# Performance work log

Hardware: AMD Instinct MI355X
Metric: run time of the kernel (lower is better)

Reference implementation:

```python
import jax, jax.numpy as jnp
import numpy as np
from jax import lax

EPS = 1e-5

def conv2d(x, w, pad, dil):
    # x: NCHW, w: OIHW
    return lax.conv_general_dilated(
        x, w, window_strides=(1, 1), padding=[(pad, pad), (pad, pad)],
        rhs_dilation=(dil, dil), dimension_numbers=("NCHW", "OIHW", "NCHW"))

def batchnorm(x, gamma, beta):
    # training-mode BN: batch statistics over (N, H, W), biased variance
    m = x.mean(axis=(0, 2, 3), keepdims=True)
    v = x.var(axis=(0, 2, 3), keepdims=True)
    xh = (x - m) * lax.rsqrt(v + EPS)
    return gamma[None, :, None, None] * xh + beta[None, :, None, None]

def maxpool2(x):
    return lax.reduce_window(x, -jnp.inf, lax.max, (1, 1, 2, 2), (1, 1, 2, 2), "VALID")

def mhsa(x, wq, bq, wk, bk, wv, bv, rel_h, rel_w, heads=1):
    B, C, H, W = x.shape
    N = H * W
    d = C // heads
    q = (conv2d(x, wq, 0, 1) + bq[None, :, None, None]).reshape(B, heads, d, N)
    k = (conv2d(x, wk, 0, 1) + bk[None, :, None, None]).reshape(B, heads, d, N)
    v = (conv2d(x, wv, 0, 1) + bv[None, :, None, None]).reshape(B, heads, d, N)
    # content-content: q^T k -> [B, h, N, N]
    cc = jnp.einsum("bhdn,bhdm->bhnm", q, k)
    # content-position: (rel_h + rel_w) reshaped to [h, d, N], transposed, times q
    pos = (rel_h + rel_w).reshape(heads, d, N)  # broadcast-sum [1,h,d,1,H]+[1,h,d,W,1]
    cp = jnp.einsum("hnd,bhdm->bhnm", jnp.swapaxes(pos, 1, 2), q)
    attn = jax.nn.softmax(cc + cp, axis=-1)
    # out = v @ attn^T
    out = jnp.einsum("bhdn,bhmn->bhdm", v, attn)
    return out.reshape(B, C, H, W)


def setup_inputs() -> dict:
    key = jax.random.key(0)
    ks = jax.random.split(key, 16)
    B, in_ch, out_ch, S = 4, 128, 256, 64
    c4 = out_ch // 4  # 64 = MHSA channel dim
    w_scale = 0.05
    inp = {
        "x": jax.random.normal(ks[0], (B, in_ch, 2 * S, 2 * S), jnp.float32),
        "dc_w1": jax.random.normal(ks[1], (out_ch, in_ch, 3, 3), jnp.float32) * w_scale,
        "dc_b1": jnp.zeros((out_ch,), jnp.float32),
        "dc_g1": jnp.ones((out_ch,), jnp.float32),
        "dc_be1": jnp.zeros((out_ch,), jnp.float32),
        "dc_w2": jax.random.normal(ks[2], (out_ch, out_ch, 3, 3), jnp.float32) * w_scale,
        "dc_b2": jnp.zeros((out_ch,), jnp.float32),
        "dc_g2": jnp.ones((out_ch,), jnp.float32),
        "dc_be2": jnp.zeros((out_ch,), jnp.float32),
        "aspp1_w": jax.random.normal(ks[3], (c4, out_ch, 1, 1), jnp.float32) * w_scale,
        "aspp1_g": jnp.ones((c4,), jnp.float32),
        "aspp1_b": jnp.zeros((c4,), jnp.float32),
        "aspp2_w": jax.random.normal(ks[4], (c4, out_ch, 3, 3), jnp.float32) * w_scale,
        "aspp2_g": jnp.ones((c4,), jnp.float32),
        "aspp2_b": jnp.zeros((c4,), jnp.float32),
        "aspp3_w": jax.random.normal(ks[5], (c4, out_ch, 3, 3), jnp.float32) * w_scale,
        "aspp3_g": jnp.ones((c4,), jnp.float32),
        "aspp3_b": jnp.zeros((c4,), jnp.float32),
        "aspp4_w": jax.random.normal(ks[6], (c4, out_ch, 3, 3), jnp.float32) * w_scale,
        "aspp4_g": jnp.ones((c4,), jnp.float32),
        "aspp4_b": jnp.zeros((c4,), jnp.float32),
        "wq": jax.random.normal(ks[7], (c4, c4, 1, 1), jnp.float32) * w_scale,
        "bq": jnp.zeros((c4,), jnp.float32),
        "wk": jax.random.normal(ks[8], (c4, c4, 1, 1), jnp.float32) * w_scale,
        "bk": jnp.zeros((c4,), jnp.float32),
        "wv": jax.random.normal(ks[9], (c4, c4, 1, 1), jnp.float32) * w_scale,
        "bv": jnp.zeros((c4,), jnp.float32),
        "rel_h": jax.random.normal(ks[10], (1, 1, c4, 1, S), jnp.float32),
        "rel_w": jax.random.normal(ks[11], (1, 1, c4, S, 1), jnp.float32),
    }
    return inp


def reference(x, dc_w1, dc_b1, dc_g1, dc_be1, dc_w2, dc_b2, dc_g2, dc_be2,
              aspp1_w, aspp1_g, aspp1_b, aspp2_w, aspp2_g, aspp2_b,
              aspp3_w, aspp3_g, aspp3_b, aspp4_w, aspp4_g, aspp4_b,
              wq, bq, wk, bk, wv, bv, rel_h, rel_w):
    dilations = (1, 3, 6, 9)
    # mpconv: MaxPool2d(2) -> double_conv
    h = maxpool2(x)
    h = jax.nn.relu(batchnorm(conv2d(h, dc_w1, 1, 1) + dc_b1[None, :, None, None], dc_g1, dc_be1))
    h = jax.nn.relu(batchnorm(conv2d(h, dc_w2, 1, 1) + dc_b2[None, :, None, None], dc_g2, dc_be2))

    aspp = [(aspp1_w, aspp1_g, aspp1_b), (aspp2_w, aspp2_g, aspp2_b),
            (aspp3_w, aspp3_g, aspp3_b), (aspp4_w, aspp4_g, aspp4_b)]
    outs = []
    for (w, g, b), dil in zip(aspp, dilations):
        pad = 0 if dil == 1 else dil
        branch = jax.nn.relu(batchnorm(conv2d(h, w, pad, dil), g, b))
        outs.append(mhsa(branch, wq, bq, wk, bk, wv, bv, rel_h, rel_w))
    return jnp.concatenate(outs, axis=1)
```

## Files before the change

### kernel.cpp

```cpp
#include <hip/hip_runtime.h>
#include <math.h>

constexpr int Bn = 4;
constexpr int S  = 64;
constexpr int N  = 4096;

#define DEV static __device__ __forceinline__

typedef __attribute__((ext_vector_type(8))) short bf16x8;
typedef __attribute__((ext_vector_type(4))) float f32x4;

DEV unsigned short bfc(float x) {
  unsigned u = __float_as_uint(x);
  unsigned r = (u + 0x7FFFu + ((u >> 16) & 1u)) >> 16;
  return (unsigned short)r;
}

DEV void fma4(float4& a, float s, const float4 u) {
  a.x = fmaf(s, u.x, a.x); a.y = fmaf(s, u.y, a.y);
  a.z = fmaf(s, u.z, a.z); a.w = fmaf(s, u.w, a.w);
}

DEV void gload_lds16(const unsigned short* g, unsigned short* l) {
  __builtin_amdgcn_global_load_lds(
      (const __attribute__((address_space(1))) void*)g,
      (__attribute__((address_space(3))) void*)l, 16, 0, 0);
}

DEV void pswap32(unsigned& a, unsigned& b) {
  asm("v_permlane32_swap_b32 %0, %1" : "+v"(a), "+v"(b));
}
DEV void pswap16(unsigned& a, unsigned& b) {
  asm("v_permlane16_swap_b32 %0, %1" : "+v"(a), "+v"(b));
}

__global__ __launch_bounds__(256) void wtr_kernel(const float* __restrict__ src,
                                                  unsigned short* __restrict__ dst,
                                                  int Cout, int Cin, int T) {
  int i = blockIdx.x * 256 + threadIdx.x;
  int ci = i % Cin;
  int r  = i / Cin;
  int t  = r / Cout;
  int co = r - t * Cout;
  dst[i] = bfc(src[((size_t)co * Cin + ci) * T + t]);
}

__global__ __launch_bounds__(256) void pool_kernel(const float* __restrict__ x,
                                                   unsigned short* __restrict__ Pp1) {
  int i = blockIdx.x * 256 + threadIdx.x;
  int xg = i & 15, y = (i >> 4) & 63, c = (i >> 10) & 127, b = i >> 17;
  const float* s = x + (((size_t)(b * 128 + c) * 128) + 2 * y) * 128 + 8 * xg;
  float4 u0 = *(const float4*)(s), u1 = *(const float4*)(s + 4);
  float4 u2 = *(const float4*)(s + 128), u3 = *(const float4*)(s + 132);
  float m0 = fmaxf(fmaxf(u0.x, u0.y), fmaxf(u2.x, u2.y));
  float m1 = fmaxf(fmaxf(u0.z, u0.w), fmaxf(u2.z, u2.w));
  float m2 = fmaxf(fmaxf(u1.x, u1.y), fmaxf(u3.x, u3.y));
  float m3 = fmaxf(fmaxf(u1.z, u1.w), fmaxf(u3.z, u3.w));
  unsigned short* d = Pp1 + (((size_t)b * 66 + y + 1) * 66 + xg * 4 + 1) * 128 + c;
  d[0] = bfc(m0); d[128] = bfc(m1); d[256] = bfc(m2); d[384] = bfc(m3);
}

template <int CTOT>
__global__ __launch_bounds__(256) void dcconv_kernel(
    const unsigned short* __restrict__ in, const unsigned short* __restrict__ wt,
    float* __restrict__ out) {
  const int Wp = 66, CSEG = CTOT / 2;
  const int w = threadIdx.x >> 6, lane = threadIdx.x & 63;
  const int ln = lane & 15, quad = lane >> 4;
  const int b = blockIdx.z >> 1, h = blockIdx.z & 1, co0 = blockIdx.y * 64;
  const int n0 = blockIdx.x * 128 + w * 32;
  const unsigned short* inb = in + (size_t)b * Wp * Wp * CTOT + h * CSEG;
  const unsigned short* wth = wt + h * CSEG;
  float* outh = out + (size_t)h * 4 * 256 * N;
  size_t pix[2];
#pragma unroll
  for (int j = 0; j < 2; j++) {
    int n = n0 + j * 16 + ln;
    int y = n >> 6, x = n & 63;
    pix[j] = ((size_t)y * Wp + x) * CTOT;
  }
  f32x4 acc[4][2];
#pragma unroll
  for (int i = 0; i < 4; i++)
#pragma unroll
    for (int j = 0; j < 2; j++) acc[i][j] = (f32x4)(0.f);
#pragma unroll
  for (int ky = 0; ky < 3; ky++)
#pragma unroll
    for (int kx = 0; kx < 3; kx++) {
      const size_t toff = ((size_t)ky * Wp + kx) * CTOT;
      const unsigned short* wtap = wth + (size_t)(ky * 3 + kx) * 256 * CTOT;
      for (int kc = 0; kc < CSEG / 32; kc++) {
        const int ko = kc * 32 + quad * 8;
        bf16x8 a[4], bb[2];
#pragma unroll
        for (int i = 0; i < 4; i++)
          a[i] = *(const bf16x8*)(wtap + (size_t)(co0 + i * 16 + ln) * CTOT + ko);
#pragma unroll
        for (int j = 0; j < 2; j++)
          bb[j] = *(const bf16x8*)(inb + pix[j] + toff + ko);
#pragma unroll
        for (int i = 0; i < 4; i++)
#pragma unroll
          for (int j = 0; j < 2; j++)
            acc[i][j] = __builtin_amdgcn_mfma_f32_16x16x32_bf16(a[i], bb[j], acc[i][j], 0, 0, 0);
      }
    }
#pragma unroll
  for (int i = 0; i < 4; i++)
#pragma unroll
    for (int j = 0; j < 2; j++)
#pragma unroll
      for (int r = 0; r < 4; r++)
        outh[((size_t)(b * 256 + co0 + i * 16 + quad * 4 + r)) * N + n0 + j * 16 + ln] =
            acc[i][j][r];
}

__global__ __launch_bounds__(256) void branch_kernel(
    const unsigned short* __restrict__ in, const unsigned short* __restrict__ wtall,
    float* __restrict__ br) {
  const int Wp = 82, halo = 9, CIN = 256;
  const int w = threadIdx.x >> 6, lane = threadIdx.x & 63;
  const int ln = lane & 15, quad = lane >> 4;
  const int bb = blockIdx.y;
  const int kbr = bb >> 2, b = bb & 3;
  const int dil = (kbr == 0) ? 1 : 3 * kbr;
  const int klo = (kbr == 0) ? 1 : 0, khi = (kbr == 0) ? 2 : 3;
  const int hd = halo - dil;
  const int cw = (w & 1) * 32, nw = (w >> 1) * 32;
  const int n0 = blockIdx.x * 64 + nw;
  const unsigned short* inb = in + (size_t)b * Wp * Wp * CIN;
  size_t pix[2];
#pragma unroll
  for (int j = 0; j < 2; j++) {
    int n = n0 + j * 16 + ln;
    int y = n >> 6, x = n & 63;
    pix[j] = ((size_t)(y + hd) * Wp + x + hd) * CIN;
  }
  f32x4 acc[2][2];
#pragma unroll
  for (int i = 0; i < 2; i++)
#pragma unroll
    for (int j = 0; j < 2; j++) acc[i][j] = (f32x4)(0.f);
  for (int ky = klo; ky < khi; ky++)
    for (int kx = klo; kx < khi; kx++) {
      const size_t toff = ((size_t)ky * Wp + kx) * dil * CIN;
      const unsigned short* wtap =
          wtall + ((size_t)kbr * 9 + ky * 3 + kx) * 64 * CIN;
      for (int kc = 0; kc < CIN / 32; kc++) {
        const int ko = kc * 32 + quad * 8;
        bf16x8 a[2], bv[2];
#pragma unroll
        for (int i = 0; i < 2; i++)
          a[i] = *(const bf16x8*)(wtap + (size_t)(cw + i * 16 + ln) * CIN + ko);
#pragma unroll
        for (int j = 0; j < 2; j++)
          bv[j] = *(const bf16x8*)(inb + pix[j] + toff + ko);
#pragma unroll
        for (int i = 0; i < 2; i++)
#pragma unroll
          for (int j = 0; j < 2; j++)
            acc[i][j] = __builtin_amdgcn_mfma_f32_16x16x32_bf16(a[i], bv[j], acc[i][j], 0, 0, 0);
      }
    }
#pragma unroll
  for (int i = 0; i < 2; i++)
#pragma unroll
    for (int j = 0; j < 2; j++)
#pragma unroll
      for (int r = 0; r < 4; r++)
        br[((size_t)bb * 64 + cw + i * 16 + quad * 4 + r) * N + n0 + j * 16 + ln] =
            acc[i][j][r];
}

__global__ __launch_bounds__(256) void bn_stats_kernel(
    const float* __restrict__ t, const float* __restrict__ gamma,
    const float* __restrict__ beta, float* __restrict__ ss, int C) {
  const int c = blockIdx.x;
  float s = 0.f, s2 = 0.f;
  for (int b = 0; b < Bn; b++) {
    const float* p = t + ((size_t)(b * C + c)) * N;
    for (int i = threadIdx.x; i < N; i += 256) {
      float v = p[i];
      s += v; s2 = fmaf(v, v, s2);
    }
  }
  for (int off = 32; off; off >>= 1) {
    s += __shfl_down(s, off, 64);
    s2 += __shfl_down(s2, off, 64);
  }
  __shared__ float rs[4], rs2[4];
  const int wid = threadIdx.x >> 6, lane = threadIdx.x & 63;
  if (lane == 0) { rs[wid] = s; rs2[wid] = s2; }
  __syncthreads();
  if (threadIdx.x == 0) {
    float S1 = rs[0] + rs[1] + rs[2] + rs[3];
    float S2 = rs2[0] + rs2[1] + rs2[2] + rs2[3];
    const float cnt = (float)(Bn * N);
    float mean = S1 / cnt;
    float var = S2 / cnt - mean * mean;
    float sc = gamma[c] * rsqrtf(var + 1e-5f);
    ss[2 * c] = sc;
    ss[2 * c + 1] = beta[c] - mean * sc;
  }
}

__global__ __launch_bounds__(256) void bn_stats2_kernel(
    const float* __restrict__ ta, const float* __restrict__ tb,
    const float* __restrict__ gamma, const float* __restrict__ beta,
    float* __restrict__ ss, int C) {
  const int c = blockIdx.x;
  float s = 0.f, s2 = 0.f;
  for (int b = 0; b < Bn; b++) {
    const size_t base = ((size_t)(b * C + c)) * N;
    for (int i = threadIdx.x; i < N; i += 256) {
      float v = ta[base + i] + tb[base + i];
      s += v; s2 = fmaf(v, v, s2);
    }
  }
  for (int off = 32; off; off >>= 1) {
    s += __shfl_down(s, off, 64);
    s2 += __shfl_down(s2, off, 64);
  }
  __shared__ float rs[4], rs2[4];
  const int wid = threadIdx.x >> 6, lane = threadIdx.x & 63;
  if (lane == 0) { rs[wid] = s; rs2[wid] = s2; }
  __syncthreads();
  if (threadIdx.x == 0) {
    float S1 = rs[0] + rs[1] + rs[2] + rs[3];
    float S2 = rs2[0] + rs2[1] + rs2[2] + rs2[3];
    const float cnt = (float)(Bn * N);
    float mean = S1 / cnt;
    float var = S2 / cnt - mean * mean;
    float sc = gamma[c] * rsqrtf(var + 1e-5f);
    ss[2 * c] = sc;
    ss[2 * c + 1] = beta[c] - mean * sc;
  }
}

__global__ __launch_bounds__(256) void bn_norm_pad2_kernel(
    const float* __restrict__ ta, const float* __restrict__ tb,
    const float* __restrict__ ss, unsigned short* __restrict__ outp,
    int Wp, int halo) {
  int i = blockIdx.x * 256 + threadIdx.x;
  int n = i & 4095, cg = (i >> 12) & 63, b = i >> 18;
  int c0 = cg * 4;
  ushort4 pk;
  float v0, v1, v2, v3;
  {
    size_t i0 = ((size_t)(b * 256 + c0 + 0)) * N + n;
    size_t i1 = i0 + N, i2 = i1 + N, i3 = i2 + N;
    v0 = fmaxf(fmaf(ta[i0] + tb[i0], ss[2 * (c0 + 0)], ss[2 * (c0 + 0) + 1]), 0.f);
    v1 = fmaxf(fmaf(ta[i1] + tb[i1], ss[2 * (c0 + 1)], ss[2 * (c0 + 1) + 1]), 0.f);
    v2 = fmaxf(fmaf(ta[i2] + tb[i2], ss[2 * (c0 + 2)], ss[2 * (c0 + 2) + 1]), 0.f);
    v3 = fmaxf(fmaf(ta[i3] + tb[i3], ss[2 * (c0 + 3)], ss[2 * (c0 + 3) + 1]), 0.f);
  }
  pk.x = bfc(v0); pk.y = bfc(v1); pk.z = bfc(v2); pk.w = bfc(v3);
  int y = n >> 6, x = n & 63;
  *(ushort4*)(outp + (((size_t)b * Wp + y + halo) * Wp + x + halo) * 256 + c0) = pk;
}

__global__ __launch_bounds__(256) void bn_norm_kernel(
    float* __restrict__ t, const float* __restrict__ ss, int Cmask) {
  int i = blockIdx.x * 256 + threadIdx.x;
  int c = (i >> 12) & Cmask;
  t[i] = fmaxf(fmaf(t[i], ss[2 * c], ss[2 * c + 1]), 0.f);
}

__global__ __launch_bounds__(256) void qkv_kernel(
    const float* __restrict__ br,
    const float* __restrict__ wq, const float* __restrict__ bq,
    const float* __restrict__ wk, const float* __restrict__ bk,
    const float* __restrict__ wv, const float* __restrict__ bvb,
    unsigned short* __restrict__ qTo, unsigned short* __restrict__ kTo,
    unsigned short* __restrict__ vbo) {
  const int bb = blockIdx.z;
  const int p = blockIdx.y >> 2, dg = blockIdx.y & 3;
  const float* w  = p == 0 ? wq : (p == 1 ? wk : wv);
  const float* bi = p == 0 ? bq : (p == 1 ? bk : bvb);
  __shared__ float wl[64 * 16];
  const int d0b = dg * 16;
  for (int i = threadIdx.x; i < 64 * 16; i += 256)
    wl[i] = w[(size_t)(d0b + (i & 15)) * 64 + (i >> 4)];
  __syncthreads();
  const int tn = threadIdx.x & 63, td = threadIdx.x >> 6;
  const int n0 = blockIdx.x * 256 + tn * 4;
  const int d0 = d0b + td * 4;
  const float* inb = br + (size_t)bb * 64 * N;
  float4 acc[4];
#pragma unroll
  for (int j = 0; j < 4; j++) {
    float bvv = bi[d0 + j];
    acc[j] = make_float4(bvv, bvv, bvv, bvv);
  }
  for (int ci = 0; ci < 64; ci++) {
    float4 u = *(const float4*)(inb + (size_t)ci * N + n0);
    float4 wv4 = *(const float4*)(wl + ci * 16 + td * 4);
    fma4(acc[0], wv4.x, u); fma4(acc[1], wv4.y, u);
    fma4(acc[2], wv4.z, u); fma4(acc[3], wv4.w, u);
  }
  const size_t slab = (size_t)bb * N * 64;
  if (p < 2) {
    unsigned short* o = (p == 0 ? qTo : kTo) + slab;
#pragma unroll
    for (int nn = 0; nn < 4; nn++) {
      ushort4 pk;
      pk.x = bfc(((const float*)&acc[0])[nn]);
      pk.y = bfc(((const float*)&acc[1])[nn]);
      pk.z = bfc(((const float*)&acc[2])[nn]);
      pk.w = bfc(((const float*)&acc[3])[nn]);
      *(ushort4*)(o + (size_t)(n0 + nn) * 64 + d0) = pk;
    }
  } else {
    unsigned short* o = vbo + slab;
#pragma unroll
    for (int j = 0; j < 4; j++) {
      ushort4 pk;
      pk.x = bfc(acc[j].x); pk.y = bfc(acc[j].y);
      pk.z = bfc(acc[j].z); pk.w = bfc(acc[j].w);
      *(ushort4*)(o + (size_t)(d0 + j) * N + n0) = pk;
    }
  }
}

__global__ __launch_bounds__(256) void posT_kernel(
    const float* __restrict__ rel_h, const float* __restrict__ rel_w,
    unsigned short* __restrict__ posT) {
  int i = blockIdx.x * 256 + threadIdx.x;
  int n = i >> 4, dq = (i & 15) * 4;
  int h = n >> 6, wc = n & 63;
  ushort4 pk;
  pk.x = bfc(rel_w[(dq + 0) * 64 + h] + rel_h[(dq + 0) * 64 + wc]);
  pk.y = bfc(rel_w[(dq + 1) * 64 + h] + rel_h[(dq + 1) * 64 + wc]);
  pk.z = bfc(rel_w[(dq + 2) * 64 + h] + rel_h[(dq + 2) * 64 + wc]);
  pk.w = bfc(rel_w[(dq + 3) * 64 + h] + rel_h[(dq + 3) * 64 + wc]);
  *(ushort4*)(posT + (size_t)n * 64 + dq) = pk;
}

__global__ __launch_bounds__(256, 3) void flash3_kernel(
    const unsigned short* __restrict__ qT, const unsigned short* __restrict__ kT,
    const unsigned short* __restrict__ posT, const unsigned short* __restrict__ vb,
    float* __restrict__ o_part, float* __restrict__ ml) {
  const int bb = blockIdx.y, split = blockIdx.z;
  const size_t slab = (size_t)bb * N * 64;
  const unsigned short* qTs = qT + slab;
  const unsigned short* kTs = kT + slab;
  const unsigned short* vbs = vb + slab;
  const int w = threadIdx.x >> 6, lane = threadIdx.x & 63;
  const int ln = lane & 15, quad = lane >> 4;
  const int m0 = blockIdx.x * 128 + w * 32;
  __shared__ __align__(16) unsigned short As[2][4][64][32];

  const unsigned short* ssrc = (w < 2) ? kTs : qTs;
  const int ksub = (w & 1) * 32 + (lane & 3) * 8;
  const int rsub = lane >> 2;
  auto stage = [&](int c0, int bufi) {
#pragma unroll
    for (int j = 0; j < 4; j++)
      gload_lds16(ssrc + (size_t)(c0 + j * 16 + rsub) * 64 + ksub,
                  &As[bufi][w][j * 16][0]);
  };

  bf16x8 bq[4][2];
#pragma unroll
  for (int s = 0; s < 4; s++) {
    const unsigned short* src = (s < 2) ? qTs : posT;
#pragma unroll
    for (int mf = 0; mf < 2; mf++)
      bq[s][mf] = *(const bf16x8*)(src + (size_t)(m0 + mf * 16 + ln) * 64 +
                                   (s & 1) * 32 + quad * 8);
  }

  float m_run[2] = {-3.0e38f, -3.0e38f}, l_run[2] = {0.f, 0.f};
  f32x4 o_acc[4][2];
#pragma unroll
  for (int dt = 0; dt < 4; dt++)
#pragma unroll
    for (int mf = 0; mf < 2; mf++) o_acc[dt][mf] = (f32x4)(0.f);

  const int cbeg = split * 1024;
  stage(cbeg, 0);
  for (int t = 0; t < 16; t++) {
    const int c0 = cbeg + t * 64;
    const int buf = t & 1;
    __syncthreads();
    if (t < 15) stage(c0 + 64, buf ^ 1);
    f32x4 st[4][2];
#pragma unroll
    for (int jt = 0; jt < 4; jt++)
#pragma unroll
      for (int mf = 0; mf < 2; mf++) st[jt][mf] = (f32x4)(0.f);
    __builtin_amdgcn_s_setprio(1);
#pragma unroll
    for (int s = 0; s < 4; s++) {
#pragma unroll
      for (int jt = 0; jt < 4; jt++) {
        bf16x8 a = *(const bf16x8*)(&As[buf][s][jt * 16 + ln][quad * 8]);
#pragma unroll
        for (int mf = 0; mf < 2; mf++)
          st[jt][mf] = __builtin_amdgcn_mfma_f32_16x16x32_bf16(a, bq[s][mf], st[jt][mf], 0, 0, 0);
      }
    }
    __builtin_amdgcn_s_setprio(0);
    unsigned P0[2][4], P1[2][4];
#pragma unroll
    for (int mf = 0; mf < 2; mf++) {
      float mx = -3.0e38f;
#pragma unroll
      for (int jt = 0; jt < 4; jt++)
#pragma unroll
        for (int r = 0; r < 4; r++) mx = fmaxf(mx, st[jt][mf][r]);
      mx = fmaxf(mx, __shfl_xor(mx, 16, 64));
      mx = fmaxf(mx, __shfl_xor(mx, 32, 64));
      const float m_new = fmaxf(m_run[mf], mx);
      const float alpha = __expf(m_run[mf] - m_new);
      float psum = 0.f;
#pragma unroll
      for (int jt = 0; jt < 4; jt++) {
        float e0 = __expf(st[jt][mf][0] - m_new);
        float e1 = __expf(st[jt][mf][1] - m_new);
        float e2 = __expf(st[jt][mf][2] - m_new);
        float e3 = __expf(st[jt][mf][3] - m_new);
        psum += (e0 + e1) + (e2 + e3);
        P0[mf][jt] = (unsigned)bfc(e0) | ((unsigned)bfc(e1) << 16);
        P1[mf][jt] = (unsigned)bfc(e2) | ((unsigned)bfc(e3) << 16);
      }
      psum += __shfl_xor(psum, 16, 64);
      psum += __shfl_xor(psum, 32, 64);
      l_run[mf] = l_run[mf] * alpha + psum;
      m_run[mf] = m_new;
#pragma unroll
      for (int dt = 0; dt < 4; dt++)
#pragma unroll
        for (int r = 0; r < 4; r++) o_acc[dt][mf][r] *= alpha;
    }
    __builtin_amdgcn_s_setprio(1);
#pragma unroll
    for (int tt = 0; tt < 2; tt++) {
      bf16x8 av[4];
#pragma unroll
      for (int dt = 0; dt < 4; dt++)
        av[dt] = *(const bf16x8*)(vbs + (size_t)(dt * 16 + ln) * N + c0 + tt * 32 + quad * 8);
#pragma unroll
      for (int mf = 0; mf < 2; mf++) {
        unsigned x0 = P0[mf][2 * tt], y0 = P0[mf][2 * tt + 1];
        pswap32(x0, y0); pswap16(x0, y0);
        unsigned x1 = P1[mf][2 * tt], y1 = P1[mf][2 * tt + 1];
        pswap32(x1, y1); pswap16(x1, y1);
        union { unsigned u[4]; bf16x8 v; } bp;
        bp.u[0] = x0; bp.u[1] = x1; bp.u[2] = y0; bp.u[3] = y1;
#pragma unroll
        for (int dt = 0; dt < 4; dt++)
          o_acc[dt][mf] = __builtin_amdgcn_mfma_f32_16x16x32_bf16(av[dt], bp.v, o_acc[dt][mf], 0, 0, 0);
      }
    }
    __builtin_amdgcn_s_setprio(0);
  }
  float* ob = o_part + ((size_t)(split * 16 + bb) * 64) * N;
#pragma unroll
  for (int dt = 0; dt < 4; dt++)
#pragma unroll
    for (int mf = 0; mf < 2; mf++)
#pragma unroll
      for (int r = 0; r < 4; r++) {
        int d = dt * 16 + quad * 4 + r;
        ob[(size_t)d * N + m0 + mf * 16 + ln] = o_acc[dt][mf][r];
      }
  if (quad == 0) {
#pragma unroll
    for (int mf = 0; mf < 2; mf++) {
      int m = m0 + mf * 16 + ln;
      ml[((size_t)(split * 16 + bb) * 2 + 0) * N + m] = m_run[mf];
      ml[((size_t)(split * 16 + bb) * 2 + 1) * N + m] = l_run[mf];
    }
  }
}

__global__ __launch_bounds__(256) void wcomb_kernel(const float* __restrict__ ml,
                                                    float* __restrict__ wcb) {
  int i = blockIdx.x * 256 + threadIdx.x;
  int m = i & 4095, bb = i >> 12;
  float mv[4], lv[4];
#pragma unroll
  for (int s = 0; s < 4; s++) {
    mv[s] = ml[((size_t)(s * 16 + bb) * 2 + 0) * N + m];
    lv[s] = ml[((size_t)(s * 16 + bb) * 2 + 1) * N + m];
  }
  float M = fmaxf(fmaxf(mv[0], mv[1]), fmaxf(mv[2], mv[3]));
  float wsc[4], denom = 0.f;
#pragma unroll
  for (int s = 0; s < 4; s++) {
    wsc[s] = __expf(mv[s] - M);
    denom = fmaf(wsc[s], lv[s], denom);
  }
  float inv = 1.0f / denom;
#pragma unroll
  for (int s = 0; s < 4; s++)
    wcb[(size_t)(s * 16 + bb) * N + m] = wsc[s] * inv;
}

__global__ __launch_bounds__(256) void comb_kernel(const float* __restrict__ o_part,
                                                   const float* __restrict__ wcb,
                                                   float* __restrict__ out) {
  int i = blockIdx.x * 256 + threadIdx.x;
  int m4 = i & 1023, d = (i >> 10) & 63, bb = i >> 16;
  int kbr = bb >> 2, b = bb & 3;
  float4 acc = make_float4(0.f, 0.f, 0.f, 0.f);
#pragma unroll
  for (int s = 0; s < 4; s++) {
    const float4 o = *(const float4*)(o_part + ((size_t)(s * 16 + bb) * 64 + d) * N + m4 * 4);
    const float4 wv = *(const float4*)(wcb + (size_t)(s * 16 + bb) * N + m4 * 4);
    acc.x = fmaf(o.x, wv.x, acc.x); acc.y = fmaf(o.y, wv.y, acc.y);
    acc.z = fmaf(o.z, wv.z, acc.z); acc.w = fmaf(o.w, wv.w, acc.w);
  }
  *(float4*)(out + ((size_t)(b * 256 + kbr * 64 + d)) * N + m4 * 4) = acc;
}

extern "C" void kernel_launch(void* const* d_in, const int* in_sizes, int n_in,
                              void* d_out, int out_size, void* d_ws, size_t ws_size,
                              hipStream_t stream) {
  const float* x      = (const float*)d_in[0];
  const float* dc_w1  = (const float*)d_in[1];
  const float* dc_g1  = (const float*)d_in[3];
  const float* dc_be1 = (const float*)d_in[4];
  const float* dc_w2  = (const float*)d_in[5];
  const float* dc_g2  = (const float*)d_in[7];
  const float* dc_be2 = (const float*)d_in[8];
  const float* aspp_w[4] = {(const float*)d_in[9],  (const float*)d_in[12],
                            (const float*)d_in[15], (const float*)d_in[18]};
  const float* aspp_g[4] = {(const float*)d_in[10], (const float*)d_in[13],
                            (const float*)d_in[16], (const float*)d_in[19]};
  const float* aspp_b[4] = {(const float*)d_in[11], (const float*)d_in[14],
                            (const float*)d_in[17], (const float*)d_in[20]};
  const float* wq = (const float*)d_in[21];
  const float* bq = (const float*)d_in[22];
  const float* wk = (const float*)d_in[23];
  const float* bk = (const float*)d_in[24];
  const float* wv = (const float*)d_in[25];
  const float* bv = (const float*)d_in[26];
  const float* rel_h = (const float*)d_in[27];
  const float* rel_w = (const float*)d_in[28];
  float* out = (float*)d_out;

  float* ws = (float*)d_ws;
  size_t off = 0;
  auto alloc = [&](size_t nf) { float* p = ws + off; off += nf; return p; };
  unsigned short* Pp1 = (unsigned short*)alloc((size_t)4 * 66 * 66 * 128 / 2 + 64);
  unsigned short* Pp2 = (unsigned short*)alloc((size_t)4 * 66 * 66 * 256 / 2 + 64);
  unsigned short* Pp3 = (unsigned short*)alloc((size_t)4 * 82 * 82 * 256 / 2 + 64);
  const size_t HALF = (size_t)4 * 256 * N;
  float* t1   = alloc(2 * HALF);
  float* br   = alloc((size_t)4 * 4 * 64 * N);
  float* st1  = alloc(512);
  float* st2  = alloc(512);
  float* sta  = alloc(512);
  unsigned short* qT    = (unsigned short*)alloc((size_t)16 * N * 64 / 2);
  unsigned short* kT    = (unsigned short*)alloc((size_t)16 * N * 64 / 2);
  unsigned short* vb    = (unsigned short*)alloc((size_t)16 * N * 64 / 2);
  unsigned short* posT  = (unsigned short*)alloc((size_t)N * 64 / 2);
  unsigned short* wt1   = (unsigned short*)alloc((size_t)9 * 256 * 128 / 2);
  unsigned short* wt2   = (unsigned short*)alloc((size_t)9 * 256 * 256 / 2);
  unsigned short* wtbr  = (unsigned short*)alloc((size_t)4 * 9 * 64 * 256 / 2);
  float* o_part = alloc((size_t)4 * 16 * 64 * N);
  float* mlb    = alloc((size_t)4 * 16 * 2 * N);
  float* wcb    = alloc((size_t)4 * 16 * N);

  hipMemsetAsync(Pp1, 0, (size_t)4 * 66 * 66 * 128 * 2, stream);
  hipMemsetAsync(Pp2, 0, (size_t)4 * 66 * 66 * 256 * 2, stream);
  hipMemsetAsync(Pp3, 0, (size_t)4 * 82 * 82 * 256 * 2, stream);
  hipMemsetAsync(wtbr, 0, (size_t)4 * 9 * 64 * 256 * 2, stream);

  wtr_kernel<<<(9 * 256 * 128) / 256, 256, 0, stream>>>(dc_w1, wt1, 256, 128, 9);
  wtr_kernel<<<(9 * 256 * 256) / 256, 256, 0, stream>>>(dc_w2, wt2, 256, 256, 9);
  wtr_kernel<<<(64 * 256) / 256, 256, 0, stream>>>(
      aspp_w[0], wtbr + (size_t)4 * 64 * 256, 64, 256, 1);
  for (int kbr = 1; kbr < 4; kbr++)
    wtr_kernel<<<(9 * 64 * 256) / 256, 256, 0, stream>>>(
        aspp_w[kbr], wtbr + (size_t)kbr * 9 * 64 * 256, 64, 256, 9);

  pool_kernel<<<2048, 256, 0, stream>>>(x, Pp1);

  dcconv_kernel<128><<<dim3(32, 4, 8), 256, 0, stream>>>(Pp1, wt1, t1);
  bn_stats2_kernel<<<256, 256, 0, stream>>>(t1, t1 + HALF, dc_g1, dc_be1, st1, 256);
  bn_norm_pad2_kernel<<<4096, 256, 0, stream>>>(t1, t1 + HALF, st1, Pp2, 66, 1);
  dcconv_kernel<256><<<dim3(32, 4, 8), 256, 0, stream>>>(Pp2, wt2, t1);
  bn_stats2_kernel<<<256, 256, 0, stream>>>(t1, t1 + HALF, dc_g2, dc_be2, st2, 256);
  bn_norm_pad2_kernel<<<4096, 256, 0, stream>>>(t1, t1 + HALF, st2, Pp3, 82, 9);

  branch_kernel<<<dim3(64, 16), 256, 0, stream>>>(Pp3, wtbr, br);
  for (int kbr = 0; kbr < 4; kbr++) {
    bn_stats_kernel<<<64, 256, 0, stream>>>(br + (size_t)kbr * 1048576,
                                            aspp_g[kbr], aspp_b[kbr],
                                            sta + kbr * 128, 64);
    bn_norm_kernel<<<4096, 256, 0, stream>>>(br + (size_t)kbr * 1048576,
                                             sta + kbr * 128, 63);
  }

  qkv_kernel<<<dim3(16, 12, 16), 256, 0, stream>>>(br, wq, bq, wk, bk, wv, bv,
                                                   qT, kT, vb);
  posT_kernel<<<256, 256, 0, stream>>>(rel_h, rel_w, posT);

  flash3_kernel<<<dim3(32, 16, 4), 256, 0, stream>>>(qT, kT, posT, vb, o_part, mlb);
  wcomb_kernel<<<256, 256, 0, stream>>>(mlb, wcb);
  comb_kernel<<<4096, 256, 0, stream>>>(o_part, wcb, out);
}
```

Baseline: 791.9 us.

## Fuse ASPP BN+ReLU into qkv, swizzle flash LDS, skip unchanged-max rescale

```diff
diff --git a/kernel.cpp b/kernel.cpp
--- a/kernel.cpp
+++ b/kernel.cpp
@@ -27,6 +27,11 @@
       (__attribute__((address_space(3))) void*)l, 16, 0, 0);
 }
 
+DEV unsigned cvtpk_bf16(float lo, float hi) {
+  unsigned r;
+  asm("v_cvt_pk_bf16_f32 %0, %1, %2" : "=v"(r) : "v"(lo), "v"(hi));
+  return r;
+}
 DEV void pswap32(unsigned& a, unsigned& b) {
   asm("v_permlane32_swap_b32 %0, %1" : "+v"(a), "+v"(b));
 }
@@ -260,15 +265,8 @@
   *(ushort4*)(outp + (((size_t)b * Wp + y + halo) * Wp + x + halo) * 256 + c0) = pk;
 }
 
-__global__ __launch_bounds__(256) void bn_norm_kernel(
-    float* __restrict__ t, const float* __restrict__ ss, int Cmask) {
-  int i = blockIdx.x * 256 + threadIdx.x;
-  int c = (i >> 12) & Cmask;
-  t[i] = fmaxf(fmaf(t[i], ss[2 * c], ss[2 * c + 1]), 0.f);
-}
-
 __global__ __launch_bounds__(256) void qkv_kernel(
-    const float* __restrict__ br,
+    const float* __restrict__ br, const float* __restrict__ sta,
     const float* __restrict__ wq, const float* __restrict__ bq,
     const float* __restrict__ wk, const float* __restrict__ bk,
     const float* __restrict__ wv, const float* __restrict__ bvb,
@@ -279,7 +277,9 @@
   const float* w  = p == 0 ? wq : (p == 1 ? wk : wv);
   const float* bi = p == 0 ? bq : (p == 1 ? bk : bvb);
   __shared__ float wl[64 * 16];
+  __shared__ float ssl[128];
   const int d0b = dg * 16;
+  if (threadIdx.x < 128) ssl[threadIdx.x] = sta[(bb >> 2) * 128 + threadIdx.x];
   for (int i = threadIdx.x; i < 64 * 16; i += 256)
     wl[i] = w[(size_t)(d0b + (i & 15)) * 64 + (i >> 4)];
   __syncthreads();
@@ -295,6 +295,11 @@
   }
   for (int ci = 0; ci < 64; ci++) {
     float4 u = *(const float4*)(inb + (size_t)ci * N + n0);
+    const float sc = ssl[2 * ci], of = ssl[2 * ci + 1];
+    u.x = fmaxf(fmaf(u.x, sc, of), 0.f);
+    u.y = fmaxf(fmaf(u.y, sc, of), 0.f);
+    u.z = fmaxf(fmaf(u.z, sc, of), 0.f);
+    u.w = fmaxf(fmaf(u.w, sc, of), 0.f);
     float4 wv4 = *(const float4*)(wl + ci * 16 + td * 4);
     fma4(acc[0], wv4.x, u); fma4(acc[1], wv4.y, u);
     fma4(acc[2], wv4.z, u); fma4(acc[3], wv4.w, u);
@@ -352,8 +357,9 @@
   __shared__ __align__(16) unsigned short As[2][4][64][32];
 
   const unsigned short* ssrc = (w < 2) ? kTs : qTs;
-  const int ksub = (w & 1) * 32 + (lane & 3) * 8;
   const int rsub = lane >> 2;
+  const int csw  = (lane & 3) ^ ((lane >> 3) & 3);
+  const int ksub = (w & 1) * 32 + csw * 8;
   auto stage = [&](int c0, int bufi) {
 #pragma unroll
     for (int j = 0; j < 4; j++)
@@ -378,6 +384,7 @@
 #pragma unroll
     for (int mf = 0; mf < 2; mf++) o_acc[dt][mf] = (f32x4)(0.f);
 
+  const int qsw = (quad ^ ((ln >> 1) & 3)) * 8;
   const int cbeg = split * 1024;
   stage(cbeg, 0);
   for (int t = 0; t < 16; t++) {
@@ -395,7 +402,7 @@
     for (int s = 0; s < 4; s++) {
 #pragma unroll
       for (int jt = 0; jt < 4; jt++) {
-        bf16x8 a = *(const bf16x8*)(&As[buf][s][jt * 16 + ln][quad * 8]);
+        bf16x8 a = *(const bf16x8*)(&As[buf][s][jt * 16 + ln][qsw]);
 #pragma unroll
         for (int mf = 0; mf < 2; mf++)
           st[jt][mf] = __builtin_amdgcn_mfma_f32_16x16x32_bf16(a, bq[s][mf], st[jt][mf], 0, 0, 0);
@@ -412,27 +419,31 @@
         for (int r = 0; r < 4; r++) mx = fmaxf(mx, st[jt][mf][r]);
       mx = fmaxf(mx, __shfl_xor(mx, 16, 64));
       mx = fmaxf(mx, __shfl_xor(mx, 32, 64));
-      const float m_new = fmaxf(m_run[mf], mx);
-      const float alpha = __expf(m_run[mf] - m_new);
+      if (!__all(mx <= m_run[mf])) {
+        const float m_new = fmaxf(m_run[mf], mx);
+        const float alpha = __expf(m_run[mf] - m_new);
+        l_run[mf] *= alpha;
+#pragma unroll
+        for (int dt = 0; dt < 4; dt++)
+#pragma unroll
+          for (int r = 0; r < 4; r++) o_acc[dt][mf][r] *= alpha;
+        m_run[mf] = m_new;
+      }
+      const float mc = m_run[mf];
       float psum = 0.f;
 #pragma unroll
       for (int jt = 0; jt < 4; jt++) {
-        float e0 = __expf(st[jt][mf][0] - m_new);
-        float e1 = __expf(st[jt][mf][1] - m_new);
-        float e2 = __expf(st[jt][mf][2] - m_new);
-        float e3 = __expf(st[jt][mf][3] - m_new);
+        float e0 = __expf(st[jt][mf][0] - mc);
+        float e1 = __expf(st[jt][mf][1] - mc);
+        float e2 = __expf(st[jt][mf][2] - mc);
+        float e3 = __expf(st[jt][mf][3] - mc);
         psum += (e0 + e1) + (e2 + e3);
-        P0[mf][jt] = (unsigned)bfc(e0) | ((unsigned)bfc(e1) << 16);
-        P1[mf][jt] = (unsigned)bfc(e2) | ((unsigned)bfc(e3) << 16);
+        P0[mf][jt] = cvtpk_bf16(e0, e1);
+        P1[mf][jt] = cvtpk_bf16(e2, e3);
       }
       psum += __shfl_xor(psum, 16, 64);
       psum += __shfl_xor(psum, 32, 64);
-      l_run[mf] = l_run[mf] * alpha + psum;
-      m_run[mf] = m_new;
-#pragma unroll
-      for (int dt = 0; dt < 4; dt++)
-#pragma unroll
-        for (int r = 0; r < 4; r++) o_acc[dt][mf][r] *= alpha;
+      l_run[mf] += psum;
     }
     __builtin_amdgcn_s_setprio(1);
 #pragma unroll
@@ -588,16 +599,13 @@
   bn_norm_pad2_kernel<<<4096, 256, 0, stream>>>(t1, t1 + HALF, st2, Pp3, 82, 9);
 
   branch_kernel<<<dim3(64, 16), 256, 0, stream>>>(Pp3, wtbr, br);
-  for (int kbr = 0; kbr < 4; kbr++) {
+  for (int kbr = 0; kbr < 4; kbr++)
     bn_stats_kernel<<<64, 256, 0, stream>>>(br + (size_t)kbr * 1048576,
                                             aspp_g[kbr], aspp_b[kbr],
                                             sta + kbr * 128, 64);
-    bn_norm_kernel<<<4096, 256, 0, stream>>>(br + (size_t)kbr * 1048576,
-                                             sta + kbr * 128, 63);
-  }
-
-  qkv_kernel<<<dim3(16, 12, 16), 256, 0, stream>>>(br, wq, bq, wk, bk, wv, bv,
-                                                   qT, kT, vb);
+
+  qkv_kernel<<<dim3(16, 12, 16), 256, 0, stream>>>(br, sta, wq, bq, wk, bk,
+                                                   wv, bv, qT, kT, vb);
   posT_kernel<<<256, 256, 0, stream>>>(rel_h, rel_w, posT);
 
   flash3_kernel<<<dim3(32, 16, 4), 256, 0, stream>>>(qT, kT, posT, vb, o_part, mlb);
```

Result: faster. 772.0 us (-2.5%).
